# Kernel optimization log

Hardware: AMD Instinct MI355X
Metric: run time of the kernel (lower is better)

The kernel has to match this reference:

```python
import jax, jax.numpy as jnp
import numpy as np

WORD = 32  # bits packed per uint32 word

def setup_inputs() -> dict:
    key = jax.random.key(0)
    # binary source values in [0,1); bit = (x > 0.5)
    x = jax.random.uniform(key, (4096, 32768), dtype=jnp.float32)
    return {"x": x}

def reference(x) -> jnp.ndarray:
    # Consolidate bits: pack every WORD consecutive binary values along the
    # last dim into one uint32 word via shift-and-OR (bit i -> position i).
    B, N = x.shape
    bits = (x > 0.5).astype(jnp.uint32).reshape(B, N // WORD, WORD)
    shifts = jnp.arange(WORD, dtype=jnp.uint32)  # [WORD]
    words = jnp.sum(bits << shifts, axis=-1, dtype=jnp.uint32)  # [B, N//WORD]
    return words
```

## Files before the change

### kernel.cpp

```cpp
#include <hip/hip_runtime.h>


__global__ __launch_bounds__(256) void ConsolidateBits_35888746725585_kernel(
    const float* __restrict__ x,
    unsigned int* __restrict__ out,
    long long n_elems) {
    const int lane = threadIdx.x & 63;
    const long long tid    = (long long)blockIdx.x * blockDim.x + threadIdx.x;
    const long long stride = (long long)gridDim.x * blockDim.x;

    for (long long e = 4 * tid; e < n_elems; e += 4 * stride) {
        const float4 v = *reinterpret_cast<const float4*>(x + e);
        unsigned int nib =
            (unsigned int)(v.x > 0.5f)        |
            ((unsigned int)(v.y > 0.5f) << 1) |
            ((unsigned int)(v.z > 0.5f) << 2) |
            ((unsigned int)(v.w > 0.5f) << 3);
        unsigned int word = nib << (4 * (lane & 7));
        word |= __shfl_xor(word, 1);
        word |= __shfl_xor(word, 2);
        word |= __shfl_xor(word, 4);
        if ((lane & 7) == 0) {
            out[e >> 5] = word;
        }
    }
}

extern "C" void kernel_launch(void* const* d_in, const int* in_sizes, int n_in,
                              void* d_out, int out_size, void* d_ws, size_t ws_size,
                              hipStream_t stream) {
    const float* x = (const float*)d_in[0];
    unsigned int* out = (unsigned int*)d_out;
    const long long n_elems = (long long)in_sizes[0];

    const int threads = 256;
    const int blocks = 2048;
    hipLaunchKernelGGL(ConsolidateBits_35888746725585_kernel,
                       dim3(blocks), dim3(threads), 0, stream,
                       x, out, n_elems);
}
```

Before: 100.3 us.

## Pack bits with wavefront ballot instead of per-thread nibbles and shuffles

Replaces the float4-per-thread load, nibble construction and three xor-shuffles with per-wave scalar loads of 512 floats, where each wave-wide ballot directly yields 64 packed bits. Eight lanes then each store one 64-bit word, so there are fewer, wider stores and the shuffle/ALU work disappears. A tail loop handles leftover elements. The trade-off is that loads become 4-byte per lane instead of 16-byte, which may reduce memory efficiency on a kernel that is already bandwidth-bound.

```diff
diff --git a/kernel.cpp b/kernel.cpp
--- a/kernel.cpp
+++ b/kernel.cpp
@@ -3,25 +3,52 @@
 
 __global__ __launch_bounds__(256) void ConsolidateBits_35888746725585_kernel(
     const float* __restrict__ x,
-    unsigned int* __restrict__ out,
-    long long n_elems) {
+    unsigned long long* __restrict__ out64,
+    long long n) {
     const int lane = threadIdx.x & 63;
-    const long long tid    = (long long)blockIdx.x * blockDim.x + threadIdx.x;
-    const long long stride = (long long)gridDim.x * blockDim.x;
+    const long long wave   = ((long long)blockIdx.x * blockDim.x + threadIdx.x) >> 6;
+    const long long nwaves = ((long long)gridDim.x * blockDim.x) >> 6;
 
-    for (long long e = 4 * tid; e < n_elems; e += 4 * stride) {
-        const float4 v = *reinterpret_cast<const float4*>(x + e);
-        unsigned int nib =
-            (unsigned int)(v.x > 0.5f)        |
-            ((unsigned int)(v.y > 0.5f) << 1) |
-            ((unsigned int)(v.z > 0.5f) << 2) |
-            ((unsigned int)(v.w > 0.5f) << 3);
-        unsigned int word = nib << (4 * (lane & 7));
-        word |= __shfl_xor(word, 1);
-        word |= __shfl_xor(word, 2);
-        word |= __shfl_xor(word, 4);
-        if ((lane & 7) == 0) {
-            out[e >> 5] = word;
+    const long long STEP = 512;
+    const long long nfull = n & ~(STEP - 1);
+
+    for (long long base = wave * STEP; base < nfull; base += nwaves * STEP) {
+        const float* p = x + base + lane;
+        float v0 = p[0];
+        float v1 = p[64];
+        float v2 = p[128];
+        float v3 = p[192];
+        float v4 = p[256];
+        float v5 = p[320];
+        float v6 = p[384];
+        float v7 = p[448];
+        unsigned long long b0 = __ballot(v0 > 0.5f);
+        unsigned long long b1 = __ballot(v1 > 0.5f);
+        unsigned long long b2 = __ballot(v2 > 0.5f);
+        unsigned long long b3 = __ballot(v3 > 0.5f);
+        unsigned long long b4 = __ballot(v4 > 0.5f);
+        unsigned long long b5 = __ballot(v5 > 0.5f);
+        unsigned long long b6 = __ballot(v6 > 0.5f);
+        unsigned long long b7 = __ballot(v7 > 0.5f);
+        if (lane < 8) {
+            unsigned long long b =
+                lane == 0 ? b0 : lane == 1 ? b1 : lane == 2 ? b2 :
+                lane == 3 ? b3 : lane == 4 ? b4 : lane == 5 ? b5 :
+                lane == 6 ? b6 : b7;
+            out64[(base >> 6) + lane] = b;
+        }
+    }
+
+    if (wave == 0) {
+        unsigned int* out32 = (unsigned int*)out64;
+        for (long long base = nfull; base < n; base += 64) {
+            long long e = base + lane;
+            bool pred = (e < n) && (x[e] > 0.5f);
+            unsigned long long b = __ballot(pred);
+            if (lane == 0) {
+                out32[base >> 5] = (unsigned int)b;
+                if (base + 32 < n) out32[(base >> 5) + 1] = (unsigned int)(b >> 32);
+            }
         }
     }
 }
@@ -30,12 +57,12 @@
                               void* d_out, int out_size, void* d_ws, size_t ws_size,
                               hipStream_t stream) {
     const float* x = (const float*)d_in[0];
-    unsigned int* out = (unsigned int*)d_out;
-    const long long n_elems = (long long)in_sizes[0];
+    unsigned long long* out64 = (unsigned long long*)d_out;
+    const long long n = (long long)in_sizes[0];
 
     const int threads = 256;
     const int blocks = 2048;
     hipLaunchKernelGGL(ConsolidateBits_35888746725585_kernel,
                        dim3(blocks), dim3(threads), 0, stream,
-                       x, out, n_elems);
+                       x, out64, n);
 }
```

New measurement: 110.6 us. +10.3%, slower.

## Use one-shot grid with DPP reductions and 64-bit packed stores

Applied to the files above, without the earlier changes.

Replaces the grid-stride loop with a one-shot grid in which each wave handles 512 elements. Each lane loads two float4s, and the 8-lane OR reduction now uses DPP moves instead of shuffles. Two 32-bit words are combined into a single 64-bit store per 8-lane group, and a ballot-based tail path covers remainders. The aim is to cut shuffle and loop overhead and halve the number of store instructions, at the cost of launching many more blocks. The second load is strided by 32 floats, which may hurt coalescing slightly.

```diff
diff --git a/kernel.cpp b/kernel.cpp
--- a/kernel.cpp
+++ b/kernel.cpp
@@ -1,27 +1,55 @@
 #include <hip/hip_runtime.h>
 
 
+typedef unsigned int u32;
+typedef unsigned long long u64;
+
+__device__ __forceinline__ u32 group8_or(u32 v) {
+    u32 t;
+    t = __builtin_amdgcn_mov_dpp(v, 0xB1, 0xF, 0xF, 1);  v |= t;
+    t = __builtin_amdgcn_mov_dpp(v, 0x4E, 0xF, 0xF, 1);  v |= t;
+    t = __builtin_amdgcn_mov_dpp(v, 0x141, 0xF, 0xF, 1); v |= t;
+    return v;
+}
+
+__device__ __forceinline__ u32 pack4(float4 v) {
+    return (u32)(v.x > 0.5f)        |
+           ((u32)(v.y > 0.5f) << 1) |
+           ((u32)(v.z > 0.5f) << 2) |
+           ((u32)(v.w > 0.5f) << 3);
+}
+
 __global__ __launch_bounds__(256) void ConsolidateBits_35888746725585_kernel(
     const float* __restrict__ x,
-    unsigned int* __restrict__ out,
-    long long n_elems) {
+    u64* __restrict__ out64,
+    long long n) {
     const int lane = threadIdx.x & 63;
-    const long long tid    = (long long)blockIdx.x * blockDim.x + threadIdx.x;
-    const long long stride = (long long)gridDim.x * blockDim.x;
+    const int k = lane >> 3;
+    const int j = lane & 7;
+    const long long wave = ((long long)blockIdx.x * blockDim.x + threadIdx.x) >> 6;
+    const long long base = wave << 9;
 
-    for (long long e = 4 * tid; e < n_elems; e += 4 * stride) {
-        const float4 v = *reinterpret_cast<const float4*>(x + e);
-        unsigned int nib =
-            (unsigned int)(v.x > 0.5f)        |
-            ((unsigned int)(v.y > 0.5f) << 1) |
-            ((unsigned int)(v.z > 0.5f) << 2) |
-            ((unsigned int)(v.w > 0.5f) << 3);
-        unsigned int word = nib << (4 * (lane & 7));
-        word |= __shfl_xor(word, 1);
-        word |= __shfl_xor(word, 2);
-        word |= __shfl_xor(word, 4);
-        if ((lane & 7) == 0) {
-            out[e >> 5] = word;
+    if (base + 512 <= n) {
+        const long long e0 = base + 64 * k + 4 * j;
+        const float4 a = *reinterpret_cast<const float4*>(x + e0);
+        const float4 b = *reinterpret_cast<const float4*>(x + e0 + 32);
+        u32 wa = pack4(a) << (4 * j);
+        u32 wb = pack4(b) << (4 * j);
+        wa = group8_or(wa);
+        wb = group8_or(wb);
+        if (j == 0) {
+            out64[(base >> 6) + k] = (u64)wa | ((u64)wb << 32);
+        }
+    } else if (base < n) {
+        u32* out32 = (u32*)out64;
+        for (long long s = base; s < n && s < base + 512; s += 64) {
+            long long e = s + lane;
+            bool p = (e < n) && (x[e] > 0.5f);
+            u64 bb = __ballot(p);
+            if (lane == 0) {
+                out32[s >> 5] = (u32)bb;
+                if (s + 32 < n) out32[(s >> 5) + 1] = (u32)(bb >> 32);
+            }
         }
     }
 }
@@ -30,12 +58,13 @@
                               void* d_out, int out_size, void* d_ws, size_t ws_size,
                               hipStream_t stream) {
     const float* x = (const float*)d_in[0];
-    unsigned int* out = (unsigned int*)d_out;
-    const long long n_elems = (long long)in_sizes[0];
+    u64* out64 = (u64*)d_out;
+    const long long n = (long long)in_sizes[0];
 
     const int threads = 256;
-    const int blocks = 2048;
+    const long long nwaves = (n + 511) >> 9;
+    const long long blocks = (nwaves + 3) >> 2;
     hipLaunchKernelGGL(ConsolidateBits_35888746725585_kernel,
-                       dim3(blocks), dim3(threads), 0, stream,
-                       x, out, n_elems);
+                       dim3((unsigned)blocks), dim3(threads), 0, stream,
+                       x, out64, n);
 }
```

Result: faster. 94.09 us (-6.2%).
